# Performance work log

Hardware: AMD Instinct MI355X
Metric: run time of the kernel (lower is better)

The kernel has to match this reference:

```python
import jax, jax.numpy as jnp
import numpy as np

N = 100000   # nodes per node type ('net' and 'cell')
E = 600000   # edges per canonical relation
D_IN = 16    # raw input feature dim
D = 128      # hidden dim (in_size == out_size, required by wl: Linear(2*D -> D))
SLOPE = 0.2  # DGL GATConv leaky_relu negative slope


def setup_inputs() -> dict:
    key = jax.random.key(0)
    ks = jax.random.split(key, 24)
    f = lambda k, shp, scale=1.0: jax.random.normal(k, shp, dtype=jnp.float32) * scale
    s_in = 1.0 / np.sqrt(D_IN).astype(np.float32)
    s_d = 1.0 / np.sqrt(D).astype(np.float32)
    s_2d = 1.0 / np.sqrt(2 * D).astype(np.float32)
    inp = {
        'x_net':   f(ks[0], (N, D_IN)),
        'x_cell':  f(ks[1], (N, D_IN)),
        'Wp_net':  f(ks[2], (D, D_IN), s_in),
        'Wp_cell': f(ks[3], (D, D_IN), s_in),
        # per-edge-type GATConv params: fc weight + attn_l + attn_r (num_heads=1, no bias)
        'Wg0': f(ks[4], (D, D), s_d), 'al0': f(ks[5], (D,), s_d), 'ar0': f(ks[6], (D,), s_d),
        'Wg1': f(ks[7], (D, D), s_d), 'al1': f(ks[8], (D,), s_d), 'ar1': f(ks[9], (D,), s_d),
        'Wg2': f(ks[10], (D, D), s_d), 'al2': f(ks[11], (D,), s_d), 'ar2': f(ks[12], (D,), s_d),
        'Wl':   f(ks[13], (D, 2 * D), s_2d),
        'bias': jnp.zeros((D,), jnp.float32),
        # edge lists: relation 0 = cell->net, 1 = net->cell, 2 = net->net
        'src0': jax.random.randint(ks[14], (E,), 0, N, dtype=jnp.int32),
        'dst0': jax.random.randint(ks[15], (E,), 0, N, dtype=jnp.int32),
        'src1': jax.random.randint(ks[16], (E,), 0, N, dtype=jnp.int32),
        'dst1': jax.random.randint(ks[17], (E,), 0, N, dtype=jnp.int32),
        'src2': jax.random.randint(ks[18], (E,), 0, N, dtype=jnp.int32),
        'dst2': jax.random.randint(ks[19], (E,), 0, N, dtype=jnp.int32),
    }
    return inp


def _gat(x_src, x_dst, W, al, ar, src, dst):
    """DGL GATConv (num_heads=1, bias=False) on one relation's edge list."""
    h_src = x_src @ W.T                               # [N, D]
    h_dst = x_dst @ W.T                               # [N, D]
    el = (h_src @ al)[src]                            # [E] gathered src logits
    er = (h_dst @ ar)[dst]                            # [E] gathered dst logits
    e = jax.nn.leaky_relu(el + er, SLOPE)             # [E]
    # segment softmax over incoming edges of each dst node
    m = jax.ops.segment_max(e, dst, num_segments=N)
    ex = jnp.exp(e - m[dst])
    denom = jax.ops.segment_sum(ex, dst, num_segments=N)
    alpha = ex / denom[dst]                           # [E]
    return jax.ops.segment_sum(h_src[src] * alpha[:, None], dst, num_segments=N)


def reference(x_net, x_cell, Wp_net, Wp_cell,
              Wg0, al0, ar0, Wg1, al1, ar1, Wg2, al2, ar2,
              Wl, bias,
              src0, dst0, src1, dst1, src2, dst2):
    # feature projection per node type (ParaGraph.feat_proj)
    h_net = x_net @ Wp_net.T                          # [N, D]
    h_cell = x_cell @ Wp_cell.T                       # [N, D]
    feat = {'net': h_net, 'cell': h_cell}
    out = {'net': jnp.zeros((N, D), h_net.dtype), 'cell': jnp.zeros((N, D), h_cell.dtype)}
    # canonical etypes: (srctype, dsttype, gat params, edge list)
    rels = [
        ('cell', 'net', Wg0, al0, ar0, src0, dst0),
        ('net', 'cell', Wg1, al1, ar1, src1, dst1),
        ('net', 'net',  Wg2, al2, ar2, src2, dst2),
    ]
    for st, dt, W, al, ar, src, dst in rels:
        out[dt] = out[dt] + _gat(feat[st], feat[dt], W, al, ar, src, dst)
        # faithful to the original: concat+linear+relu recomputed for EVERY ntype
        # inside the etype loop (the redundant fused-op pattern)
        for nt in ('net', 'cell'):
            out[nt] = jax.nn.relu(
                jnp.concatenate([feat[nt], out[nt] + bias], axis=1) @ Wl.T)
    return jnp.stack([out['net'], out['cell']])      # [2, N, D]
```

## Files before the change

kernel.cpp:

```cpp
#include <hip/hip_runtime.h>
#include <hip/hip_bf16.h>
#include <stdint.h>

#define NN 100000
#define NE 600000
#define SP 136
#define NB 782
#define BCAP 1600
#define CHUNK 4096
#define NCH 147
#define GB 1563
#define AB 6250

typedef unsigned short u16;
typedef unsigned int u32;
typedef __attribute__((ext_vector_type(8))) short short8;
typedef __attribute__((ext_vector_type(8))) __bf16 bf16x8;
typedef __attribute__((ext_vector_type(4))) float floatx4;

__device__ __forceinline__ float b2f(u16 u) {
  union { float f; u32 i; } c; c.i = ((u32)u) << 16; return c.f;
}
__device__ __forceinline__ u16 f2b(float f) {
  union { float f; u32 i; } c; c.f = f;
  u32 r = c.i + 0x7FFFu + ((c.i >> 16) & 1u);
  return (u16)(r >> 16);
}


__device__ __forceinline__ void gemm_w(const u16* __restrict__ W, int ldw, u16* __restrict__ C,
                                       u16* lds, int tid, int row0, const bf16x8* a,
                                       int m16, int quad, int wv) {
#pragma unroll
  for (int it = 0; it < 8; ++it) {
    int idx = it * 256 + tid;
    int r = idx >> 4, c = (idx & 15) << 3;
    *(short8*)(&lds[r * SP + c]) = *(const short8*)(W + (size_t)r * ldw + c);
  }
  __syncthreads();
  const u16* brow = &lds[m16 * SP + quad * 8];
  floatx4 acc[8];
#pragma unroll
  for (int c = 0; c < 8; ++c) acc[c] = floatx4{0.f, 0.f, 0.f, 0.f};
#pragma unroll
  for (int kk = 0; kk < 4; ++kk) {
#pragma unroll
    for (int c = 0; c < 8; ++c) {
      bf16x8 bfr = *(const bf16x8*)(brow + c * 16 * SP + kk * 32);
      acc[c] = __builtin_amdgcn_mfma_f32_16x16x32_bf16(a[kk], bfr, acc[c], 0, 0, 0);
    }
  }
#pragma unroll
  for (int c = 0; c < 8; ++c) {
    int col = c * 16 + m16;
#pragma unroll
    for (int r = 0; r < 4; ++r) {
      int grow = row0 + wv * 16 + quad * 4 + r;
      if (grow < NN) C[(size_t)grow * 128 + col] = f2b(acc[c][r]);
    }
  }
}

__device__ __forceinline__ void stageW2(const u16* __restrict__ W2, u16* Wlds, int tid) {
#pragma unroll
  for (int it = 0; it < 8; ++it) {
    int idx = it * 256 + tid;
    int r = idx >> 4, c = (idx & 15) << 3;
    *(short8*)(&Wlds[r * SP + c]) = *(const short8*)(W2 + (size_t)r * 256 + c);
  }
}

template<int INIT>
__device__ __forceinline__ void gat_phase(int nb, int tid, const u16* __restrict__ h,
                                          const u32* __restrict__ srecs, const int* __restrict__ rp,
                                          const float* __restrict__ el, const float* __restrict__ er,
                                          u16* Alds) {
  int sub = tid & 15, g = tid >> 4;
  int n = nb * 16 + g;
  int start = rp[n], end = rp[n + 1];
  float row[8];
  if (INIT) {
    short8 pv = *(const short8*)(&Alds[g * SP + sub * 8]);
#pragma unroll
    for (int t = 0; t < 8; ++t) row[t] = b2f((u16)pv[t]);
  } else {
#pragma unroll
    for (int t = 0; t < 8; ++t) row[t] = 0.f;
  }
  if (start < end) {
    float ern = er[n];
    float acc[8];
#pragma unroll
    for (int t = 0; t < 8; ++t) acc[t] = 0.f;
    float sl = 0.f;
    const u16* hsub = h + sub * 8;
    for (int base = start; base < end; base += 16) {
      int m = end - base; if (m > 16) m = 16;
      int srci = 0; float w = 0.f;
      if (sub < m) {
        srci = (int)srecs[base + sub];
        float l = el[srci] + ern;
        l = (l >= 0.f) ? l : 0.2f * l;
        w = __expf(l);
      }
      sl += w;
      for (int i = 0; i < m; ++i) {
        float x = __shfl(w, i, 16);
        int sv = __shfl(srci, i, 16);
        short8 hv = *(const short8*)(hsub + (size_t)sv * 128);
#pragma unroll
        for (int t = 0; t < 8; ++t) acc[t] += x * b2f((u16)hv[t]);
      }
    }
    float s = sl;
#pragma unroll
    for (int off = 8; off > 0; off >>= 1) s += __shfl_xor(s, off, 16);
    float inv = 1.f / s;
#pragma unroll
    for (int t = 0; t < 8; ++t) row[t] += acc[t] * inv;
  }
  short8 rb;
#pragma unroll
  for (int t = 0; t < 8; ++t) rb[t] = (short)f2b(row[t]);
  *(short8*)(&Alds[g * SP + sub * 8]) = rb;
}

template<int TO_GLOBAL>
__device__ __forceinline__ void F_phase(int nb, int tid, const u16* __restrict__ P,
                                        const float* __restrict__ cvec,
                                        const u16* Wlds, u16* Alds, void* __restrict__ out) {
  const int lane = tid & 63, wv = tid >> 6;
  const int m16 = lane & 15, quad = lane >> 4;
  const u16* arow = &Alds[m16 * SP + quad * 8];
  bf16x8 a[4];
#pragma unroll
  for (int kk = 0; kk < 4; ++kk) a[kk] = *(const bf16x8*)(arow + kk * 32);
  if (!TO_GLOBAL) __syncthreads();
  const u16* brow = &Wlds[m16 * SP + quad * 8];
  floatx4 acc2[2];
#pragma unroll
  for (int cc = 0; cc < 2; ++cc) acc2[cc] = floatx4{0.f, 0.f, 0.f, 0.f};
#pragma unroll
  for (int kk = 0; kk < 4; ++kk) {
#pragma unroll
    for (int cc = 0; cc < 2; ++cc) {
      int ct = wv * 2 + cc;
      bf16x8 bfr = *(const bf16x8*)(brow + ct * 16 * SP + kk * 32);
      acc2[cc] = __builtin_amdgcn_mfma_f32_16x16x32_bf16(a[kk], bfr, acc2[cc], 0, 0, 0);
    }
  }
#pragma unroll
  for (int cc = 0; cc < 2; ++cc) {
    int ct = wv * 2 + cc;
    int col = ct * 16 + m16;
    float cv = cvec[col];
#pragma unroll
    for (int r = 0; r < 4; ++r) {
      int nrow = quad * 4 + r;
      int node = nb * 16 + nrow;
      float v = acc2[cc][r] + b2f(P[(size_t)node * 128 + col]) + cv;
      v = fmaxf(v, 0.f);
      if (TO_GLOBAL) ((float*)out)[(size_t)node * 128 + col] = v;
      else           Alds[nrow * SP + col] = f2b(v);
    }
  }
  if (!TO_GLOBAL) __syncthreads();
}


__global__ __launch_bounds__(256) void prep_k(const float* __restrict__ x_net, const float* __restrict__ x_cell,
                                              const float* __restrict__ Wp_net, const float* __restrict__ Wp_cell,
                                              u16* __restrict__ feat_net, u16* __restrict__ feat_cell,
                                              const float* __restrict__ Wl, const float* __restrict__ Wg0,
                                              const float* __restrict__ Wg1, const float* __restrict__ Wg2,
                                              u16* __restrict__ Wl_bf, u16* __restrict__ Wg_bf,
                                              const float* al0, const float* ar0, const float* al1,
                                              const float* ar1, const float* al2, const float* ar2,
                                              const float* bias, float* __restrict__ vecs,
                                              int* __restrict__ bcnt) {
  int bid = blockIdx.x, tid = threadIdx.x;
  if (bid < 2 * AB) {
    int y = bid >= AB;
    int bx = y ? bid - AB : bid;
    const float* x  = y ? x_cell : x_net;
    const float* Wp = y ? Wp_cell : Wp_net;
    u16* feat       = y ? feat_cell : feat_net;
    __shared__ float Ws[128 * 17];
    __shared__ float xs[16][17];
#pragma unroll
    for (int it = 0; it < 8; ++it) {
      int idx = it * 256 + tid;
      int j = idx >> 4, k = idx & 15;
      Ws[j * 17 + k] = Wp[idx];
    }
    int n0 = bx * 16;
    { int nn = tid >> 4, k = tid & 15;
      xs[nn][k] = x[(size_t)(n0 + nn) * 16 + k]; }
    __syncthreads();
    int j = tid & 127, g = tid >> 7;
    float acc[8];
#pragma unroll
    for (int r = 0; r < 8; ++r) acc[r] = 0.f;
#pragma unroll
    for (int k = 0; k < 16; ++k) {
      float w = Ws[j * 17 + k];
#pragma unroll
      for (int r = 0; r < 8; ++r) acc[r] += xs[g * 8 + r][k] * w;
    }
#pragma unroll
    for (int r = 0; r < 8; ++r)
      feat[(size_t)(n0 + g * 8 + r) * 128 + j] = f2b(acc[r]);
  } else if (bid < 2 * AB + 128) {
    int cid = bid - 2 * AB;
    int y = cid >> 5, bx = cid & 31;
    const float* src = (y == 0) ? Wl : (y == 1) ? Wg0 : (y == 2) ? Wg1 : Wg2;
    u16* dst = (y == 0) ? Wl_bf : Wg_bf + (size_t)(y - 1) * 16384;
    int n = (y == 0) ? 32768 : 16384;
    int i = (bx * 256 + tid) * 4;
    if (i >= n) return;
    float4 v = *(const float4*)(src + i);
    ushort4 p; p.x = f2b(v.x); p.y = f2b(v.y); p.z = f2b(v.z); p.w = f2b(v.w);
    *(ushort4*)(dst + i) = p;
  } else if (bid < 2 * AB + 135) {
    int a = bid - (2 * AB + 128);
    if (tid >= 128) return;
    int j = tid;
    float s = 0.f;
    if (a < 6) {
      const float* W = (a < 2) ? Wg0 : (a < 4) ? Wg1 : Wg2;
      const float* v = (a == 0) ? al0 : (a == 1) ? ar0 : (a == 2) ? al1 : (a == 3) ? ar1 : (a == 4) ? al2 : ar2;
      for (int i = 0; i < 128; ++i) s += W[i * 128 + j] * v[i];
    } else {
      for (int i = 0; i < 128; ++i) s += Wl[(size_t)j * 256 + 128 + i] * bias[i];
    }
    vecs[a * 128 + j] = s;
  } else {
    int r = bid - (2 * AB + 135);
    for (int i = tid; i < NB; i += 256) bcnt[(size_t)r * NB + i] = 0;
  }
}

__global__ __launch_bounds__(256) void logbh_k(const u16* __restrict__ feat_net, const u16* __restrict__ feat_cell,
                                               const float* __restrict__ vecs, float* __restrict__ outs,
                                               const int* __restrict__ dst0, const int* __restrict__ dst1,
                                               const int* __restrict__ dst2, int* __restrict__ bcnt) {
  __shared__ int sm[NB];
  int bid = blockIdx.x, tid = threadIdx.x;
  if (bid < 782) {
    float* vs = (float*)sm;
#pragma unroll
    for (int it = 0; it < 3; ++it) vs[it * 256 + tid] = vecs[it * 256 + tid];
    __syncthreads();
    int y = bid >= 391;
    int bx = y ? bid - 391 : bid;
    const u16* f = y ? feat_cell : feat_net;
    int n = bx * 256 + tid;
    if (n >= NN) return;
    const u16* row = f + (size_t)n * 128;
    if (y == 0) {
      float s1 = 0.f, s2 = 0.f, s4 = 0.f, s5 = 0.f;
#pragma unroll
      for (int k = 0; k < 128; k += 8) {
        short8 u = *(const short8*)(row + k);
#pragma unroll
        for (int t = 0; t < 8; ++t) {
          float fv = b2f((u16)u[t]);
          s1 += fv * vs[1 * 128 + k + t]; s2 += fv * vs[2 * 128 + k + t];
          s4 += fv * vs[4 * 128 + k + t]; s5 += fv * vs[5 * 128 + k + t];
        }
      }
      outs[(size_t)1 * NN + n] = s1; outs[(size_t)2 * NN + n] = s2;
      outs[(size_t)4 * NN + n] = s4; outs[(size_t)5 * NN + n] = s5;
    } else {
      float s0 = 0.f, s3 = 0.f;
#pragma unroll
      for (int k = 0; k < 128; k += 8) {
        short8 u = *(const short8*)(row + k);
#pragma unroll
        for (int t = 0; t < 8; ++t) {
          float fv = b2f((u16)u[t]);
          s0 += fv * vs[0 * 128 + k + t]; s3 += fv * vs[3 * 128 + k + t];
        }
      }
      outs[(size_t)0 * NN + n] = s0; outs[(size_t)3 * NN + n] = s3;
    }
  } else {
    int e = bid - 782;
    int r = e / NCH, bx = e % NCH;
    const int* dst = (r == 0) ? dst0 : (r == 1) ? dst1 : dst2;
    for (int i = tid; i < NB; i += 256) sm[i] = 0;
    __syncthreads();
    int e0 = bx * CHUNK;
    int cnt = NE - e0; if (cnt > CHUNK) cnt = CHUNK;
    for (int i = tid; i < cnt; i += 256) atomicAdd(&sm[((u32)dst[e0 + i]) >> 7], 1);
    __syncthreads();
    for (int b = tid; b < NB; b += 256) {
      int c = sm[b];
      if (c) atomicAdd(&bcnt[(size_t)r * NB + b], c);
    }
  }
}

__global__ __launch_bounds__(1024) void bscan_k(const int* __restrict__ bcnt, int* __restrict__ bptr,
                                                int* __restrict__ bcur) {
  int r = blockIdx.x, t = threadIdx.x;
  const int* c = bcnt + (size_t)r * NB;
  int* p = bptr + (size_t)r * (NB + 1);
  int* cur = bcur + (size_t)r * NB;
  int v = (t < NB) ? c[t] : 0;
  __shared__ int ss[1024];
  ss[t] = v; __syncthreads();
  for (int off = 1; off < 1024; off <<= 1) {
    int u = (t >= off) ? ss[t - off] : 0;
    __syncthreads();
    ss[t] += u;
    __syncthreads();
  }
  if (t < NB) { int e = ss[t] - v; p[t] = e; cur[t] = e; }
  if (t == 1023) p[NB] = ss[1023];
}

__global__ __launch_bounds__(256) void bscatter_k(const int* __restrict__ src0, const int* __restrict__ dst0,
                                                  const int* __restrict__ src1, const int* __restrict__ dst1,
                                                  const int* __restrict__ src2, const int* __restrict__ dst2,
                                                  int* __restrict__ bcur, u32* __restrict__ recs) {
  int r = blockIdx.y;
  const int* src = (r == 0) ? src0 : (r == 1) ? src1 : src2;
  const int* dst = (r == 0) ? dst0 : (r == 1) ? dst1 : dst2;
  __shared__ int hist[NB];
  __shared__ int lstart[NB];
  __shared__ int lcur[NB];
  __shared__ int badj[NB];
  __shared__ u32 rbuf[CHUNK];
  __shared__ u16 kbuf[CHUNK];
  __shared__ int ss[256];
  int tid = threadIdx.x;
  int e0 = blockIdx.x * CHUNK;
  int cnt = NE - e0; if (cnt > CHUNK) cnt = CHUNK;

  for (int i = tid; i < NB; i += 256) hist[i] = 0;
  __syncthreads();
  for (int i = tid; i < cnt; i += 256) atomicAdd(&hist[((u32)dst[e0 + i]) >> 7], 1);
  __syncthreads();
  int loc[4]; int s = 0;
  int base4 = tid * 4;
#pragma unroll
  for (int j = 0; j < 4; ++j) {
    int idx = base4 + j;
    int v = (idx < NB) ? hist[idx] : 0;
    loc[j] = s; s += v;
  }
  ss[tid] = s; __syncthreads();
  for (int off = 1; off < 256; off <<= 1) {
    int u = (tid >= off) ? ss[tid - off] : 0;
    __syncthreads();
    ss[tid] += u;
    __syncthreads();
  }
  int ex = ss[tid] - s;
#pragma unroll
  for (int j = 0; j < 4; ++j) {
    int idx = base4 + j;
    if (idx < NB) { int e = ex + loc[j]; lstart[idx] = e; lcur[idx] = e; }
  }
  __syncthreads();
  for (int b = tid; b < NB; b += 256) {
    int c = hist[b];
    int g = 0;
    if (c) g = atomicAdd(&bcur[(size_t)r * NB + b], c);
    badj[b] = g - lstart[b];
  }
  __syncthreads();
  for (int i = tid; i < cnt; i += 256) {
    int dN = dst[e0 + i], sN = src[e0 + i];
    int b = ((u32)dN) >> 7;
    int pos = atomicAdd(&lcur[b], 1);
    rbuf[pos] = ((u32)(dN & 127) << 17) | (u32)sN;
    kbuf[pos] = (u16)b;
  }
  __syncthreads();
  u32* out = recs + (size_t)r * NE;
  for (int i = tid; i < cnt; i += 256) {
    int b = kbuf[i];
    out[badj[b] + i] = rbuf[i];
  }
}

__global__ __launch_bounds__(256) void sortgemm_k(u32* __restrict__ recs, const int* __restrict__ bptr,
                                                  int* __restrict__ rowptr,
                                                  const u16* __restrict__ feat_net, const u16* __restrict__ feat_cell,
                                                  const u16* __restrict__ Wl_bf, const u16* __restrict__ Wg_bf,
                                                  u16* __restrict__ P_net, u16* __restrict__ P_cell,
                                                  u16* __restrict__ h0, u16* __restrict__ h1, u16* __restrict__ h2) {
  __shared__ u32 smem[128 * SP / 2];
  int bid = blockIdx.x, tid = threadIdx.x;
  if (bid < 2 * GB) {
    int ntype = bid >= GB;
    int blk = ntype ? bid - GB : bid;
    u16* lds = (u16*)smem;
    const u16* A = ntype ? feat_cell : feat_net;
    const int row0 = blk * 64;
    const int lane = tid & 63, wv = tid >> 6;
    const int m16 = lane & 15, quad = lane >> 4;
    int arow = row0 + wv * 16 + m16;
    if (arow >= NN) arow = NN - 1;
    const u16* Ab = A + (size_t)arow * 128 + quad * 8;
    bf16x8 a[4];
#pragma unroll
    for (int kk = 0; kk < 4; ++kk) a[kk] = *(const bf16x8*)(Ab + kk * 32);
    if (!ntype) {
      gemm_w(Wl_bf,          256, P_net, lds, tid, row0, a, m16, quad, wv);
      __syncthreads();
      gemm_w(Wg_bf + 16384,  128, h1,    lds, tid, row0, a, m16, quad, wv);
      __syncthreads();
      gemm_w(Wg_bf + 32768,  128, h2,    lds, tid, row0, a, m16, quad, wv);
    } else {
      gemm_w(Wl_bf,          256, P_cell, lds, tid, row0, a, m16, quad, wv);
      __syncthreads();
      gemm_w(Wg_bf,          128, h0,     lds, tid, row0, a, m16, quad, wv);
    }
  } else {
    int sb = bid - 2 * GB;
    int r = sb / NB, b = sb % NB;
    const int* p = bptr + (size_t)r * (NB + 1);
    u32* rec = recs + (size_t)r * NE;
    int* rp = rowptr + (size_t)r * (NN + 1);
    int base = p[b], end = p[b + 1];
    int cnt = end - base; if (cnt > BCAP) cnt = BCAP;
    u32* rs = smem;
    int* hist = (int*)(smem + BCAP);
    int* excl = hist + 128;
    int* cur  = excl + 128;
    for (int i = tid; i < cnt; i += 256) rs[i] = rec[base + i];
    if (tid < 128) hist[tid] = 0;
    __syncthreads();
    for (int i = tid; i < cnt; i += 256) atomicAdd(&hist[rs[i] >> 17], 1);
    __syncthreads();
    if (tid < 128) cur[tid] = hist[tid];
    __syncthreads();
    for (int off = 1; off < 128; off <<= 1) {
      int v = 0;
      if (tid < 128 && tid >= off) v = cur[tid - off];
      __syncthreads();
      if (tid < 128) cur[tid] += v;
      __syncthreads();
    }
    if (tid < 128) {
      int e = cur[tid] - hist[tid];
      excl[tid] = e;
      int node = b * 128 + tid;
      if (node < NN) rp[node] = base + e;
    }
    if (b == NB - 1 && tid == 0) rp[NN] = p[NB];
    if (tid < 128) cur[tid] = excl[tid];
    __syncthreads();
    for (int i = tid; i < cnt; i += 256) {
      u32 v = rs[i];
      int pos = atomicAdd(&cur[v >> 17], 1);
      rec[base + pos] = v & 0x1FFFFu;
    }
  }
}

__global__ __launch_bounds__(256) void tail_k(const u16* __restrict__ h0, const u16* __restrict__ h1,
                                              const u16* __restrict__ h2,
                                              const u32* __restrict__ recs, const int* __restrict__ rowptr,
                                              const float* __restrict__ logit,
                                              const u16* __restrict__ P_net, const u16* __restrict__ P_cell,
                                              const u16* __restrict__ W2, const float* __restrict__ cvec,
                                              float* __restrict__ out_net, float* __restrict__ out_cell) {
  __shared__ u16 Wlds[128 * SP];
  __shared__ u16 Alds[16 * SP];
  int bid = blockIdx.x, tid = threadIdx.x;
  stageW2(W2, Wlds, tid);
  if (bid < AB) {
    int nb = bid;
    gat_phase<0>(nb, tid, h0, recs, rowptr, logit, logit + (size_t)NN, Alds);
    __syncthreads();
    F_phase<0>(nb, tid, P_net, cvec, Wlds, Alds, nullptr);
    F_phase<0>(nb, tid, P_net, cvec, Wlds, Alds, nullptr);
    gat_phase<1>(nb, tid, h2, recs + (size_t)2 * NE, rowptr + 2 * (NN + 1),
                 logit + (size_t)4 * NN, logit + (size_t)5 * NN, Alds);
    __syncthreads();
    F_phase<1>(nb, tid, P_net, cvec, Wlds, Alds, (void*)out_net);
  } else {
    int nb = bid - AB;
    {
      int sub = tid & 15, g = tid >> 4;
      int n = nb * 16 + g;
      short8 pv = *(const short8*)(P_cell + (size_t)n * 128 + sub * 8);
      short8 rb;
#pragma unroll
      for (int t = 0; t < 8; ++t)
        rb[t] = (short)f2b(fmaxf(b2f((u16)pv[t]) + cvec[sub * 8 + t], 0.f));
      *(short8*)(&Alds[g * SP + sub * 8]) = rb;
    }
    gat_phase<1>(nb, tid, h1, recs + (size_t)NE, rowptr + (NN + 1),
                 logit + (size_t)2 * NN, logit + (size_t)3 * NN, Alds);
    __syncthreads();
    F_phase<0>(nb, tid, P_cell, cvec, Wlds, Alds, nullptr);
    F_phase<1>(nb, tid, P_cell, cvec, Wlds, Alds, (void*)out_cell);
  }
}

extern "C" void kernel_launch(void* const* d_in, const int* in_sizes, int n_in,
                              void* d_out, int out_size, void* d_ws, size_t ws_size,
                              hipStream_t stream) {
  const float* x_net   = (const float*)d_in[0];
  const float* x_cell  = (const float*)d_in[1];
  const float* Wp_net  = (const float*)d_in[2];
  const float* Wp_cell = (const float*)d_in[3];
  const float* Wg[3] = {(const float*)d_in[4], (const float*)d_in[7], (const float*)d_in[10]};
  const float* al[3] = {(const float*)d_in[5], (const float*)d_in[8], (const float*)d_in[11]};
  const float* ar[3] = {(const float*)d_in[6], (const float*)d_in[9], (const float*)d_in[12]};
  const float* Wl    = (const float*)d_in[13];
  const float* bias  = (const float*)d_in[14];
  const int* src[3] = {(const int*)d_in[15], (const int*)d_in[17], (const int*)d_in[19]};
  const int* dst[3] = {(const int*)d_in[16], (const int*)d_in[18], (const int*)d_in[20]};

  char* ws = (char*)d_ws;
  size_t off = 0;
  auto alloc = [&](size_t b) { void* p = ws + off; off = (off + b + 255) & ~(size_t)255; return p; };
  u16*  feat_net  = (u16*)alloc((size_t)NN * 128 * 2);
  u16*  feat_cell = (u16*)alloc((size_t)NN * 128 * 2);
  u16*  hbuf0     = (u16*)alloc((size_t)NN * 128 * 2);
  u16*  hbuf1     = (u16*)alloc((size_t)NN * 128 * 2);
  u16*  hbuf2     = (u16*)alloc((size_t)NN * 128 * 2);
  u16*  P_net     = (u16*)alloc((size_t)NN * 128 * 2);
  u16*  P_cell    = (u16*)alloc((size_t)NN * 128 * 2);
  float* vecs     = (float*)alloc(7 * 128 * 4);
  float* logit    = (float*)alloc((size_t)6 * NN * 4);
  u16*   Wl_bf    = (u16*)alloc((size_t)128 * 256 * 2);
  u16*   Wg_bf    = (u16*)alloc((size_t)3 * 128 * 128 * 2);
  int*   bcnt     = (int*)alloc((size_t)3 * NB * 4);
  int*   bcur     = (int*)alloc((size_t)3 * NB * 4);
  int*   bptr     = (int*)alloc((size_t)3 * (NB + 1) * 4);
  int*   rowptr   = (int*)alloc((size_t)3 * (NN + 1) * 4);
  u32*   recs     = (u32*)alloc((size_t)3 * NE * 4);

  float* out_f = (float*)d_out;
  const u16* W2 = Wl_bf + 128;
  const float* cvec = vecs + 6 * 128;

  prep_k<<<2 * AB + 138, 256, 0, stream>>>(x_net, x_cell, Wp_net, Wp_cell, feat_net, feat_cell,
                                           Wl, Wg[0], Wg[1], Wg[2], Wl_bf, Wg_bf,
                                           al[0], ar[0], al[1], ar[1], al[2], ar[2], bias, vecs, bcnt);
  logbh_k<<<782 + 3 * NCH, 256, 0, stream>>>(feat_net, feat_cell, vecs, logit,
                                             dst[0], dst[1], dst[2], bcnt);
  bscan_k<<<3, 1024, 0, stream>>>(bcnt, bptr, bcur);
  bscatter_k<<<dim3(NCH, 3), 256, 0, stream>>>(src[0], dst[0], src[1], dst[1], src[2], dst[2],
                                               bcur, recs);
  sortgemm_k<<<2 * GB + 3 * NB, 256, 0, stream>>>(recs, bptr, rowptr, feat_net, feat_cell,
                                                  Wl_bf, Wg_bf, P_net, P_cell, hbuf0, hbuf1, hbuf2);
  tail_k<<<2 * AB, 256, 0, stream>>>(hbuf0, hbuf1, hbuf2, recs, rowptr, logit,
                                     P_net, P_cell, W2, cvec,
                                     out_f, out_f + (size_t)NN * 128);
}
```

Before: 433.6 us.

## Precompute normalized edge attention weights during bucket sort, simplify GAT aggregation

Moves the edge softmax (leaky_relu, exp, per-destination sum and reciprocal) into the per-bucket sort pass of sortgemm_k, writing normalized per-edge alpha alongside the sorted source indices. The tail kernel's gather loop then reads the precomputed alpha directly, with no shuffles or reduction, and unrolls by four edges to expose more independent row loads. This removes the el/er gathers and exp work from the latency-bound tail. In exchange it adds an extra 3*NE float array written and re-read, plus shared-memory float atomics in the sort blocks.

```diff
diff --git a/kernel.cpp b/kernel.cpp
--- a/kernel.cpp
+++ b/kernel.cpp
@@ -72,9 +72,9 @@
 
 template<int INIT>
 __device__ __forceinline__ void gat_phase(int nb, int tid, const u16* __restrict__ h,
-                                          const u32* __restrict__ srecs, const int* __restrict__ rp,
-                                          const float* __restrict__ el, const float* __restrict__ er,
-                                          u16* Alds) {
+                                          const u32* __restrict__ srecs,
+                                          const float* __restrict__ walpha,
+                                          const int* __restrict__ rp, u16* Alds) {
   int sub = tid & 15, g = tid >> 4;
   int n = nb * 16 + g;
   int start = rp[n], end = rp[n + 1];
@@ -88,36 +88,35 @@
     for (int t = 0; t < 8; ++t) row[t] = 0.f;
   }
   if (start < end) {
-    float ern = er[n];
     float acc[8];
 #pragma unroll
     for (int t = 0; t < 8; ++t) acc[t] = 0.f;
-    float sl = 0.f;
     const u16* hsub = h + sub * 8;
-    for (int base = start; base < end; base += 16) {
-      int m = end - base; if (m > 16) m = 16;
-      int srci = 0; float w = 0.f;
-      if (sub < m) {
-        srci = (int)srecs[base + sub];
-        float l = el[srci] + ern;
-        l = (l >= 0.f) ? l : 0.2f * l;
-        w = __expf(l);
+    int e = start;
+    for (; e + 4 <= end; e += 4) {
+      int s0 = (int)srecs[e],     s1 = (int)srecs[e + 1];
+      int s2 = (int)srecs[e + 2], s3 = (int)srecs[e + 3];
+      float x0 = walpha[e],     x1 = walpha[e + 1];
+      float x2 = walpha[e + 2], x3 = walpha[e + 3];
+      short8 h0 = *(const short8*)(hsub + (size_t)s0 * 128);
+      short8 h1 = *(const short8*)(hsub + (size_t)s1 * 128);
+      short8 h2 = *(const short8*)(hsub + (size_t)s2 * 128);
+      short8 h3 = *(const short8*)(hsub + (size_t)s3 * 128);
+#pragma unroll
+      for (int t = 0; t < 8; ++t) {
+        acc[t] += x0 * b2f((u16)h0[t]) + x1 * b2f((u16)h1[t])
+                + x2 * b2f((u16)h2[t]) + x3 * b2f((u16)h3[t]);
       }
-      sl += w;
-      for (int i = 0; i < m; ++i) {
-        float x = __shfl(w, i, 16);
-        int sv = __shfl(srci, i, 16);
-        short8 hv = *(const short8*)(hsub + (size_t)sv * 128);
-#pragma unroll
-        for (int t = 0; t < 8; ++t) acc[t] += x * b2f((u16)hv[t]);
-      }
-    }
-    float s = sl;
-#pragma unroll
-    for (int off = 8; off > 0; off >>= 1) s += __shfl_xor(s, off, 16);
-    float inv = 1.f / s;
-#pragma unroll
-    for (int t = 0; t < 8; ++t) row[t] += acc[t] * inv;
+    }
+    for (; e < end; ++e) {
+      int sv = (int)srecs[e];
+      float x = walpha[e];
+      short8 hv = *(const short8*)(hsub + (size_t)sv * 128);
+#pragma unroll
+      for (int t = 0; t < 8; ++t) acc[t] += x * b2f((u16)hv[t]);
+    }
+#pragma unroll
+    for (int t = 0; t < 8; ++t) row[t] += acc[t];
   }
   short8 rb;
 #pragma unroll
@@ -391,7 +390,8 @@
                                                   const u16* __restrict__ feat_net, const u16* __restrict__ feat_cell,
                                                   const u16* __restrict__ Wl_bf, const u16* __restrict__ Wg_bf,
                                                   u16* __restrict__ P_net, u16* __restrict__ P_cell,
-                                                  u16* __restrict__ h0, u16* __restrict__ h1, u16* __restrict__ h2) {
+                                                  u16* __restrict__ h0, u16* __restrict__ h1, u16* __restrict__ h2,
+                                                  const float* __restrict__ logit, float* __restrict__ walpha) {
   __shared__ u32 smem[128 * SP / 2];
   int bid = blockIdx.x, tid = threadIdx.x;
   if (bid < 2 * GB) {
@@ -424,17 +424,37 @@
     int r = sb / NB, b = sb % NB;
     const int* p = bptr + (size_t)r * (NB + 1);
     u32* rec = recs + (size_t)r * NE;
+    float* wal = walpha + (size_t)r * NE;
     int* rp = rowptr + (size_t)r * (NN + 1);
+    const float* el = logit + (size_t)(2 * r) * NN;
+    const float* er = logit + (size_t)(2 * r + 1) * NN;
     int base = p[b], end = p[b + 1];
     int cnt = end - base; if (cnt > BCAP) cnt = BCAP;
     u32* rs = smem;
-    int* hist = (int*)(smem + BCAP);
+    float* xs = (float*)(smem + BCAP);
+    int* hist = (int*)(smem + 2 * BCAP);
     int* excl = hist + 128;
     int* cur  = excl + 128;
+    float* den = (float*)(cur + 128);
+    float* ers = den + 128;
     for (int i = tid; i < cnt; i += 256) rs[i] = rec[base + i];
-    if (tid < 128) hist[tid] = 0;
-    __syncthreads();
-    for (int i = tid; i < cnt; i += 256) atomicAdd(&hist[rs[i] >> 17], 1);
+    if (tid < 128) {
+      hist[tid] = 0;
+      den[tid] = 0.f;
+      int node = b * 128 + tid;
+      ers[tid] = (node < NN) ? er[node] : 0.f;
+    }
+    __syncthreads();
+    for (int i = tid; i < cnt; i += 256) {
+      u32 v = rs[i];
+      int d = v >> 17;
+      float l = el[v & 0x1FFFFu] + ers[d];
+      l = (l >= 0.f) ? l : 0.2f * l;
+      float x = __expf(l);
+      xs[i] = x;
+      atomicAdd(&den[d], x);
+      atomicAdd(&hist[d], 1);
+    }
     __syncthreads();
     if (tid < 128) cur[tid] = hist[tid];
     __syncthreads();
@@ -450,22 +470,26 @@
       excl[tid] = e;
       int node = b * 128 + tid;
       if (node < NN) rp[node] = base + e;
+      float dd = den[tid];
+      den[tid] = (dd > 0.f) ? 1.f / dd : 0.f;
     }
     if (b == NB - 1 && tid == 0) rp[NN] = p[NB];
     if (tid < 128) cur[tid] = excl[tid];
     __syncthreads();
     for (int i = tid; i < cnt; i += 256) {
       u32 v = rs[i];
-      int pos = atomicAdd(&cur[v >> 17], 1);
+      int d = v >> 17;
+      int pos = atomicAdd(&cur[d], 1);
       rec[base + pos] = v & 0x1FFFFu;
+      wal[base + pos] = xs[i] * den[d];
     }
   }
 }
 
 __global__ __launch_bounds__(256) void tail_k(const u16* __restrict__ h0, const u16* __restrict__ h1,
                                               const u16* __restrict__ h2,
-                                              const u32* __restrict__ recs, const int* __restrict__ rowptr,
-                                              const float* __restrict__ logit,
+                                              const u32* __restrict__ recs, const float* __restrict__ walpha,
+                                              const int* __restrict__ rowptr,
                                               const u16* __restrict__ P_net, const u16* __restrict__ P_cell,
                                               const u16* __restrict__ W2, const float* __restrict__ cvec,
                                               float* __restrict__ out_net, float* __restrict__ out_cell) {
@@ -475,12 +499,12 @@
   stageW2(W2, Wlds, tid);
   if (bid < AB) {
     int nb = bid;
-    gat_phase<0>(nb, tid, h0, recs, rowptr, logit, logit + (size_t)NN, Alds);
+    gat_phase<0>(nb, tid, h0, recs, walpha, rowptr, Alds);
     __syncthreads();
     F_phase<0>(nb, tid, P_net, cvec, Wlds, Alds, nullptr);
     F_phase<0>(nb, tid, P_net, cvec, Wlds, Alds, nullptr);
-    gat_phase<1>(nb, tid, h2, recs + (size_t)2 * NE, rowptr + 2 * (NN + 1),
-                 logit + (size_t)4 * NN, logit + (size_t)5 * NN, Alds);
+    gat_phase<1>(nb, tid, h2, recs + (size_t)2 * NE, walpha + (size_t)2 * NE,
+                 rowptr + 2 * (NN + 1), Alds);
     __syncthreads();
     F_phase<1>(nb, tid, P_net, cvec, Wlds, Alds, (void*)out_net);
   } else {
@@ -495,8 +519,8 @@
         rb[t] = (short)f2b(fmaxf(b2f((u16)pv[t]) + cvec[sub * 8 + t], 0.f));
       *(short8*)(&Alds[g * SP + sub * 8]) = rb;
     }
-    gat_phase<1>(nb, tid, h1, recs + (size_t)NE, rowptr + (NN + 1),
-                 logit + (size_t)2 * NN, logit + (size_t)3 * NN, Alds);
+    gat_phase<1>(nb, tid, h1, recs + (size_t)NE, walpha + (size_t)NE,
+                 rowptr + (NN + 1), Alds);
     __syncthreads();
     F_phase<0>(nb, tid, P_cell, cvec, Wlds, Alds, nullptr);
     F_phase<1>(nb, tid, P_cell, cvec, Wlds, Alds, (void*)out_cell);
@@ -537,6 +561,7 @@
   int*   bptr     = (int*)alloc((size_t)3 * (NB + 1) * 4);
   int*   rowptr   = (int*)alloc((size_t)3 * (NN + 1) * 4);
   u32*   recs     = (u32*)alloc((size_t)3 * NE * 4);
+  float* walpha   = (float*)alloc((size_t)3 * NE * 4);
 
   float* out_f = (float*)d_out;
   const u16* W2 = Wl_bf + 128;
@@ -551,8 +576,9 @@
   bscatter_k<<<dim3(NCH, 3), 256, 0, stream>>>(src[0], dst[0], src[1], dst[1], src[2], dst[2],
                                                bcur, recs);
   sortgemm_k<<<2 * GB + 3 * NB, 256, 0, stream>>>(recs, bptr, rowptr, feat_net, feat_cell,
-                                                  Wl_bf, Wg_bf, P_net, P_cell, hbuf0, hbuf1, hbuf2);
-  tail_k<<<2 * AB, 256, 0, stream>>>(hbuf0, hbuf1, hbuf2, recs, rowptr, logit,
+                                                  Wl_bf, Wg_bf, P_net, P_cell, hbuf0, hbuf1, hbuf2,
+                                                  logit, walpha);
+  tail_k<<<2 * AB, 256, 0, stream>>>(hbuf0, hbuf1, hbuf2, recs, walpha, rowptr,
                                      P_net, P_cell, W2, cvec,
                                      out_f, out_f + (size_t)NN * 128);
 }
```

New measurement: 423.4 us, median of 2. -2.4%, faster.
